# Kernel tuning notes

Hardware: AMD Instinct MI355X
Metric: run time of the kernel (lower is better)

The kernel has to match this reference:

```python
import jax, jax.numpy as jnp
import numpy as np

N_WORDS, MAX_CHARS = 32768, 16
WORD_DIM, CHAR_DIM, HIDDEN = 256, 64, 256
VOCAB = 256


def setup_inputs() -> dict:
    key = jax.random.key(0)
    ks = jax.random.split(key, 10)
    char_indices = jax.random.randint(ks[0], (N_WORDS, MAX_CHARS), 0, VOCAB)
    char_lengths = jax.random.randint(ks[1], (N_WORDS,), 1, MAX_CHARS + 1)
    word_emb = jax.random.normal(ks[2], (N_WORDS, WORD_DIM), dtype=jnp.float32)
    s = 0.05
    E_char = jax.random.normal(ks[3], (VOCAB, CHAR_DIM), dtype=jnp.float32) * s
    W_ih = jax.random.normal(ks[4], (4 * HIDDEN, CHAR_DIM), dtype=jnp.float32) * s
    W_hh = jax.random.normal(ks[5], (4 * HIDDEN, HIDDEN), dtype=jnp.float32) * s
    b_ih = jax.random.normal(ks[6], (4 * HIDDEN,), dtype=jnp.float32) * s
    b_hh = jax.random.normal(ks[7], (4 * HIDDEN,), dtype=jnp.float32) * s
    W_lin = jax.random.normal(ks[8], (WORD_DIM, WORD_DIM + HIDDEN), dtype=jnp.float32) * s
    b_lin = jax.random.normal(ks[9], (WORD_DIM,), dtype=jnp.float32) * s
    return dict(char_indices=char_indices, char_lengths=char_lengths,
                word_emb=word_emb, E_char=E_char, W_ih=W_ih, W_hh=W_hh,
                b_ih=b_ih, b_hh=b_hh, W_lin=W_lin, b_lin=b_lin)


def _lstm_last_hidden(x, lengths, W_ih, W_hh, b_ih, b_hh):
    # x: [N, T, E]; returns final hidden h at position length-1 per row.
    N, T, _ = x.shape
    H = W_hh.shape[1]
    x_proj = jnp.einsum('nte,ge->ntg', x, W_ih) + (b_ih + b_hh)  # [N, T, 4H]
    x_proj = jnp.transpose(x_proj, (1, 0, 2))                    # time-major [T, N, 4H]

    def step(carry, inp):
        h, c = carry
        xg, t = inp
        gates = xg + h @ W_hh.T
        i, f, g, o = jnp.split(gates, 4, axis=-1)
        i, f, o = jax.nn.sigmoid(i), jax.nn.sigmoid(f), jax.nn.sigmoid(o)
        g = jnp.tanh(g)
        c_new = f * c + i * g
        h_new = o * jnp.tanh(c_new)
        mask = (t < lengths)[:, None]  # freeze state past each word's length
        h = jnp.where(mask, h_new, h)
        c = jnp.where(mask, c_new, c)
        return (h, c), None

    h0 = jnp.zeros((N, H), dtype=x.dtype)
    c0 = jnp.zeros((N, H), dtype=x.dtype)
    (h, _), _ = jax.lax.scan(step, (h0, c0), (x_proj, jnp.arange(T)))
    return h


def reference(char_indices, char_lengths, word_emb, E_char, W_ih, W_hh,
              b_ih, b_hh, W_lin, b_lin):
    char_embedded = E_char[char_indices]                        # [N, T, E]
    h = _lstm_last_hidden(char_embedded, char_lengths, W_ih, W_hh, b_ih, b_hh)
    combined = jnp.concatenate([word_emb, h], axis=-1)          # [N, WORD+H]
    return jax.nn.relu(combined @ W_lin.T + b_lin)              # [N, WORD]
```

## Files before the change

### kernel.cpp

```cpp
#include <hip/hip_runtime.h>


#define NW 32768

typedef __attribute__((ext_vector_type(8))) short short8;
typedef __attribute__((ext_vector_type(4))) float f32x4;
typedef __attribute__((ext_vector_type(4))) int i32x4;
typedef __attribute__((ext_vector_type(4))) unsigned short u16x4;

#define MFMA16(a,b,c) __builtin_amdgcn_mfma_f32_16x16x32_bf16(a,b,c,0,0,0)
#define MFMAI8(a,b,c) __builtin_amdgcn_mfma_i32_16x16x32_i8(a,b,c,0,0,0)

#define O_ORDER 0
#define O_SLEN  131072
#define O_WPK   262144
#define O_USTP  524288
#define O_WLIN  528384
#define O_PX    790528
#define O_BH    1314816
#define O_BASE  1323008

__device__ inline unsigned short f2b(float f) {
  unsigned u = __builtin_bit_cast(unsigned, f);
  u = u + 0x7fffu + ((u >> 16) & 1u);
  return (unsigned short)(u >> 16);
}
__device__ inline float b2f(unsigned short u) {
  return __builtin_bit_cast(float, ((unsigned)u) << 16);
}
__device__ inline float fsigm(float x) {
  float e = __builtin_amdgcn_exp2f(-1.44269504f * x);
  return __builtin_amdgcn_rcpf(1.0f + e);
}
__device__ inline float ftanh(float x) {
  float e = __builtin_amdgcn_exp2f(2.88539008f * x);
  return 1.0f - 2.0f * __builtin_amdgcn_rcpf(e + 1.0f);
}

__global__ void k_prep0(const float* __restrict__ whh, unsigned char* __restrict__ ws) {
  int i = blockIdx.x * 256 + threadIdx.x;
  const f32x4* r4 = (const f32x4*)(whh + i * 256);
  float mx = 0.f;
  #pragma unroll 8
  for (int k4 = 0; k4 < 64; ++k4) {
    f32x4 v = r4[k4];
    mx = fmaxf(mx, fmaxf(fmaxf(fabsf(v[0]), fabsf(v[1])),
                         fmaxf(fabsf(v[2]), fabsf(v[3]))));
  }
  ((float*)(ws + O_USTP))[i] = mx / (127.f * 127.f);
}

__global__ void k_prep1(const float* __restrict__ whh, const float* __restrict__ wlin,
                        unsigned char* __restrict__ ws) {
  int i = blockIdx.x * 256 + threadIdx.x;
  if (i < 262144) {
    int j = i & 7, lane = (i >> 3) & 63, t2 = i >> 9;
    int nt = t2 & 7, u2 = t2 >> 3;
    int kb = u2 & 7, w = u2 >> 3;
    int n = (nt >> 1) * 256 + w * 32 + (nt & 1) * 16 + (lane & 15);
    int k = kb * 32 + (lane >> 4) * 8 + j;
    float v = whh[n * 256 + k];
    float ustep = ((const float*)(ws + O_USTP))[n] * 127.f;
    float qf = (ustep > 0.f) ? v / ustep : 0.f;
    int q = (int)__builtin_rintf(qf);
    q = q < -127 ? -127 : (q > 127 ? 127 : q);
    ((signed char*)(ws + O_WPK))[i] = (signed char)q;
    return;
  }
  int i2 = i - 262144;
  {
    int j = i2 & 7, lane = (i2 >> 3) & 63, t3 = i2 >> 9;
    int kf = t3 & 15, nn = t3 >> 4;
    int n = (nn >> 2) * 64 + (nn & 3) * 16 + (lane & 15);
    int k = kf * 32 + (lane >> 4) * 8 + j;
    ((unsigned short*)(ws + O_WLIN))[i2] = f2b(wlin[n * 512 + k]);
  }
}

__global__ void k_prep2(const float* __restrict__ wih, const float* __restrict__ ech,
                        const float* __restrict__ bih, const float* __restrict__ bhh,
                        unsigned char* __restrict__ ws) {
  int id = blockIdx.x * 256 + threadIdx.x;
  int c = id >> 10, n = id & 1023;
  const f32x4* w4 = (const f32x4*)(wih + n * 64);
  const f32x4* e4 = (const f32x4*)(ech + c * 64);
  float acc = bih[n] + bhh[n];
  #pragma unroll
  for (int k4 = 0; k4 < 16; ++k4) {
    f32x4 a = w4[k4], e = e4[k4];
    acc += a[0] * e[0] + a[1] * e[1] + a[2] * e[2] + a[3] * e[3];
  }
  ((unsigned short*)(ws + O_PX))[((c << 8) + (n & 255)) * 4 + (n >> 8)] = f2b(acc);
}

__global__ void k_hist(const int* __restrict__ lens, unsigned char* __restrict__ ws) {
  __shared__ int h[16];
  int t = threadIdx.x, b = blockIdx.x;
  if (t < 16) h[t] = 0;
  __syncthreads();
  int wid = b * 256 + t;
  int l = lens[wid]; l = l < 1 ? 1 : (l > 16 ? 16 : l);
  atomicAdd(&h[l - 1], 1);
  __syncthreads();
  if (t < 16) ((int*)(ws + O_BH))[b * 16 + t] = h[t];
}

__global__ void k_scan(unsigned char* __restrict__ ws) {
  __shared__ int tot[16], g[16];
  int t = threadIdx.x;
  const int* bh = (const int*)(ws + O_BH);
  int* base = (int*)(ws + O_BASE);
  if (t < 16) {
    int s = 0;
    for (int b = 0; b < 128; ++b) s += bh[b * 16 + t];
    tot[t] = s;
  }
  __syncthreads();
  if (t == 0) { int a = 0; for (int i = 0; i < 16; ++i) { g[i] = a; a += tot[i]; } }
  __syncthreads();
  if (t < 16) {
    int run = g[t];
    for (int b = 0; b < 128; ++b) { base[b * 16 + t] = run; run += bh[b * 16 + t]; }
  }
}

__global__ void k_scatter(const int* __restrict__ lens, unsigned char* __restrict__ ws) {
  __shared__ int cnt[16];
  int t = threadIdx.x, b = blockIdx.x;
  if (t < 16) cnt[t] = 0;
  __syncthreads();
  int wid = b * 256 + t;
  int l = lens[wid]; l = l < 1 ? 1 : (l > 16 ? 16 : l);
  int rank = atomicAdd(&cnt[l - 1], 1);
  int p = ((const int*)(ws + O_BASE))[b * 16 + (l - 1)] + rank;
  ((int*)(ws + O_ORDER))[p] = wid;
  ((int*)(ws + O_SLEN))[p] = l;
}

__global__ __launch_bounds__(512)
__attribute__((amdgpu_waves_per_eu(2, 2)))
void k_main(
    const int* __restrict__ cidx, const float* __restrict__ wemb,
    const float* __restrict__ blin, float* __restrict__ outp,
    const unsigned char* __restrict__ ws) {
  extern __shared__ signed char smem[];
  signed char (*WL)[8][8][64][8] = (signed char (*)[8][8][64][8])smem;
  signed char (*Xb)[8][64][8] = (signed char (*)[8][64][8])(smem + 131072);
  int (*CW)[16] = (int (*)[16])(smem + 131072 + 16384);

  const int tid = threadIdx.x, b = blockIdx.x;
  const int w = tid >> 6, lane = tid & 63;
  const int q = lane >> 4, l15 = lane & 15;

  const int* order = (const int*)(ws + O_ORDER);
  const int* slen  = (const int*)(ws + O_SLEN);
  const signed char* wpk = (const signed char*)(ws + O_WPK);
  const float* upt = (const float*)(ws + O_USTP);
  const unsigned short* wlin = (const unsigned short*)(ws + O_WLIN);
  const unsigned short* pxt = (const unsigned short*)(ws + O_PX);

  long wreg[4][8];
  #pragma unroll
  for (int kb = 0; kb < 4; ++kb)
    #pragma unroll
    for (int nt = 0; nt < 8; ++nt)
      wreg[kb][nt] = *(const long*)(wpk + (((w * 8 + kb) * 8 + nt) * 64 + lane) * 8);

  {
    long* wlds = (long*)smem;
    const long* wsrc = (const long*)wpk;
    #pragma unroll
    for (int ii = 0; ii < 32; ++ii) {
      int f = ii * 512 + tid;
      int lane_ = f & 63, r = f >> 6;
      int nt_ = r & 7, r2 = r >> 3;
      int w_ = r2 & 7, kb4 = r2 >> 3;
      wlds[f] = wsrc[((w_ * 8 + 4 + kb4) * 8 + nt_) * 64 + lane_];
    }
  }

  float uq[8];
  #pragma unroll
  for (int nt = 0; nt < 8; ++nt) {
    int n = (nt >> 1) * 256 + w * 32 + (nt & 1) * 16 + l15;
    uq[nt] = upt[n];
  }
  const int hd0 = w * 32 + l15;
  const int mh = w >> 2, nw = w & 3;
  float blv[4];
  #pragma unroll
  for (int nt = 0; nt < 4; ++nt) blv[nt] = blin[nw * 64 + nt * 16 + l15];

  for (int sl = 0; sl < 2; ++sl) {
    const int s = sl ? (511 - b) : b;
    const int base = 64 * s;
    __syncthreads();
    {
      long* p = (long*)&Xb[0][0][0][0];
      #pragma unroll
      for (int ii = 0; ii < 4; ++ii) p[tid + 512 * ii] = 0L;
    }
    if (tid < 256) {
      int m = tid >> 2, part = tid & 3;
      int wid = order[base + m];
      *(i32x4*)&CW[m][part * 4] =
          __builtin_nontemporal_load((const i32x4*)(cidx + wid * 16 + part * 4));
    }
    int tmax[4]; unsigned lenpk[4];
    #pragma unroll
    for (int mt = 0; mt < 4; ++mt) {
      int pbm = base + 16 * mt;
      tmax[mt] = slen[pbm + 15];
      unsigned l0 = (unsigned)slen[pbm + q * 4 + 0];
      unsigned l1 = (unsigned)slen[pbm + q * 4 + 1];
      unsigned l2 = (unsigned)slen[pbm + q * 4 + 2];
      unsigned l3 = (unsigned)slen[pbm + q * 4 + 3];
      lenpk[mt] = l0 | (l1 << 8) | (l2 << 16) | (l3 << 24);
    }
    const int Tm = tmax[3];
    __syncthreads();

    float creg[4][2][4];
    unsigned hreg[4][2];
    #pragma unroll
    for (int mt = 0; mt < 4; ++mt)
      #pragma unroll
      for (int hs = 0; hs < 2; ++hs) {
        hreg[mt][hs] = 0u;
        #pragma unroll
        for (int r = 0; r < 4; ++r) creg[mt][hs][r] = 0.f;
      }

    for (int t = 0; t < Tm; ++t) {
      #pragma unroll
      for (int mt = 0; mt < 4; ++mt) {
        if (mt != 3 && t >= tmax[mt]) continue;
        long Ar[8];
        #pragma unroll
        for (int kb = 0; kb < 8; ++kb)
          Ar[kb] = *(const long*)&Xb[mt][kb][lane][0];
        int cc[4];
        #pragma unroll
        for (int r = 0; r < 4; ++r) cc[r] = CW[mt * 16 + q * 4 + r][t] & 255;
        #pragma unroll
        for (int hs = 0; hs < 2; ++hs) {
          u16x4 pb[4];
          #pragma unroll
          for (int r = 0; r < 4; ++r)
            pb[r] = *(const u16x4*)&pxt[((cc[r] << 8) + hd0 + hs * 16) * 4];
          i32x4 a0 = (i32x4)0, a1 = (i32x4)0, a2 = (i32x4)0, a3 = (i32x4)0;
          #pragma unroll
          for (int kb = 0; kb < 4; ++kb) {
            a0 = MFMAI8(Ar[kb], wreg[kb][0 + hs], a0);
            a1 = MFMAI8(Ar[kb], wreg[kb][2 + hs], a1);
            a2 = MFMAI8(Ar[kb], wreg[kb][4 + hs], a2);
            a3 = MFMAI8(Ar[kb], wreg[kb][6 + hs], a3);
          }
          #pragma unroll
          for (int kb = 4; kb < 8; ++kb) {
            long b0 = *(const long*)&WL[kb - 4][w][0 + hs][lane][0];
            long b1 = *(const long*)&WL[kb - 4][w][2 + hs][lane][0];
            long b2 = *(const long*)&WL[kb - 4][w][4 + hs][lane][0];
            long b3 = *(const long*)&WL[kb - 4][w][6 + hs][lane][0];
            a0 = MFMAI8(Ar[kb], b0, a0);
            a1 = MFMAI8(Ar[kb], b1, a1);
            a2 = MFMAI8(Ar[kb], b2, a2);
            a3 = MFMAI8(Ar[kb], b3, a3);
          }
          unsigned hp = 0;
          #pragma unroll
          for (int r = 0; r < 4; ++r) {
            float gi = (float)a0[r] * uq[0 + hs] + b2f(pb[r][0]);
            float gf = (float)a1[r] * uq[2 + hs] + b2f(pb[r][1]);
            float gg = (float)a2[r] * uq[4 + hs] + b2f(pb[r][2]);
            float go = (float)a3[r] * uq[6 + hs] + b2f(pb[r][3]);
            float si = fsigm(gi), sf = fsigm(gf);
            float sg = ftanh(gg), so = fsigm(go);
            float cold = creg[mt][hs][r];
            float cn = sf * cold + si * sg;
            float hn = so * ftanh(cn);
            int lene = (int)((lenpk[mt] >> (8 * r)) & 255u);
            bool live = t < lene;
            creg[mt][hs][r] = live ? cn : cold;
            int hq = (int)__builtin_rintf(127.f * hn);
            unsigned ob = (hreg[mt][hs] >> (8 * r)) & 255u;
            unsigned nb = live ? ((unsigned)hq & 255u) : ob;
            hp |= nb << (8 * r);
          }
          hreg[mt][hs] = hp;
        }
      }
      __syncthreads();

      #pragma unroll
      for (int mt = 0; mt < 4; ++mt) {
        if (mt != 3 && t >= tmax[mt]) continue;
        #pragma unroll
        for (int hs = 0; hs < 2; ++hs) {
          int row16 = 16 * (hs * 2 + (l15 >> 3));
          #pragma unroll
          for (int r = 0; r < 4; ++r)
            Xb[mt][w][(q * 4 + r) + row16][l15 & 7] =
                (signed char)((hreg[mt][hs] >> (8 * r)) & 255u);
        }
      }
      __syncthreads();
    }

    int widA[2];
    #pragma unroll
    for (int mi = 0; mi < 2; ++mi) widA[mi] = order[base + (2 * mh + mi) * 16 + l15];
    f32x4 fac[2][4];
    #pragma unroll
    for (int mi = 0; mi < 2; ++mi)
      #pragma unroll
      for (int nt = 0; nt < 4; ++nt) fac[mi][nt] = 0.0f;

    #pragma unroll
    for (int kf = 0; kf < 16; ++kf) {
      short8 Bn[4];
      #pragma unroll
      for (int nt = 0; nt < 4; ++nt)
        Bn[nt] = ((const short8*)wlin)[((nw * 4 + nt) * 16 + kf) * 64 + lane];
      short8 Am[2];
      #pragma unroll
      for (int mi = 0; mi < 2; ++mi) {
        if (kf < 8) {
          const f32x4* pa = (const f32x4*)(wemb + widA[mi] * 256 + kf * 32 + q * 8);
          f32x4 f0 = __builtin_nontemporal_load(pa);
          f32x4 f1 = __builtin_nontemporal_load(pa + 1);
          short8 A;
          A[0] = (short)f2b(f0[0]); A[1] = (short)f2b(f0[1]);
          A[2] = (short)f2b(f0[2]); A[3] = (short)f2b(f0[3]);
          A[4] = (short)f2b(f1[0]); A[5] = (short)f2b(f1[1]);
          A[6] = (short)f2b(f1[2]); A[7] = (short)f2b(f1[3]);
          Am[mi] = A;
        } else {
          int mtv = 2 * mh + mi;
          long ch = *(const long*)&Xb[mtv][kf - 8][lane][0];
          short8 A;
          #pragma unroll
          for (int j = 0; j < 8; ++j) {
            int v = (int)(signed char)((ch >> (8 * j)) & 255);
            A[j] = (short)f2b((float)v * (1.f / 127.f));
          }
          Am[mi] = A;
        }
      }
      #pragma unroll
      for (int mi = 0; mi < 2; ++mi)
        #pragma unroll
        for (int nt = 0; nt < 4; ++nt)
          fac[mi][nt] = MFMA16(Am[mi], Bn[nt], fac[mi][nt]);
    }
    #pragma unroll
    for (int mi = 0; mi < 2; ++mi) {
      #pragma unroll
      for (int r = 0; r < 4; ++r) {
        int wid = order[base + (2 * mh + mi) * 16 + q * 4 + r];
        float* po = outp + wid * 256 + nw * 64 + l15;
        #pragma unroll
        for (int nt = 0; nt < 4; ++nt) {
          float v = fac[mi][nt][r] + blv[nt];
          __builtin_nontemporal_store(v > 0.f ? v : 0.f, po + nt * 16);
        }
      }
    }
  }
}

extern "C" void kernel_launch(void* const* d_in, const int* in_sizes, int n_in,
                              void* d_out, int out_size, void* d_ws, size_t ws_size,
                              hipStream_t stream) {
  const int*   cidx = (const int*)d_in[0];
  const int*   clen = (const int*)d_in[1];
  const float* wemb = (const float*)d_in[2];
  const float* ech  = (const float*)d_in[3];
  const float* wih  = (const float*)d_in[4];
  const float* whh  = (const float*)d_in[5];
  const float* bih  = (const float*)d_in[6];
  const float* bhh  = (const float*)d_in[7];
  const float* wlin = (const float*)d_in[8];
  const float* blin = (const float*)d_in[9];
  float* outp = (float*)d_out;
  unsigned char* ws = (unsigned char*)d_ws;

  k_prep0<<<4, 256, 0, stream>>>(whh, ws);
  k_prep1<<<1536, 256, 0, stream>>>(whh, wlin, ws);
  k_prep2<<<1024, 256, 0, stream>>>(wih, ech, bih, bhh, ws);
  k_hist<<<128, 256, 0, stream>>>(clen, ws);
  k_scan<<<1, 64, 0, stream>>>(ws);
  k_scatter<<<128, 256, 0, stream>>>(clen, ws);
  k_main<<<256, 512, 151552, stream>>>(cidx, wemb, blin, outp, ws);
}
```

Before: 399.1 us.

## Split LSTM hidden columns across 16 waves with 1024-thread blocks

Doubles the main kernel's block to 1024 threads (16 waves), with each wave handling 16 hidden units instead of 32. Per-wave recurrent weights in registers, cell state and MFMA work are halved, and the final linear layer is split so each wave handles one 16-row slice. The aim is more latency hiding in the serial recurrence. In exchange, the per-timestep barriers now synchronise more waves, and the per-step X tile is loaded from LDS by twice as many waves.

```diff
diff --git a/kernel.cpp b/kernel.cpp
--- a/kernel.cpp
+++ b/kernel.cpp
@@ -137,8 +137,7 @@
   ((int*)(ws + O_SLEN))[p] = l;
 }
 
-__global__ __launch_bounds__(512)
-__attribute__((amdgpu_waves_per_eu(2, 2)))
+__global__ __launch_bounds__(1024)
 void k_main(
     const int* __restrict__ cidx, const float* __restrict__ wemb,
     const float* __restrict__ blin, float* __restrict__ outp,
@@ -151,6 +150,7 @@
   const int tid = threadIdx.x, b = blockIdx.x;
   const int w = tid >> 6, lane = tid & 63;
   const int q = lane >> 4, l15 = lane & 15;
+  const int wo = w >> 1, wp = w & 1;
 
   const int* order = (const int*)(ws + O_ORDER);
   const int* slen  = (const int*)(ws + O_SLEN);
@@ -159,19 +159,20 @@
   const unsigned short* wlin = (const unsigned short*)(ws + O_WLIN);
   const unsigned short* pxt = (const unsigned short*)(ws + O_PX);
 
-  long wreg[4][8];
+  long wreg[4][4];
   #pragma unroll
   for (int kb = 0; kb < 4; ++kb)
     #pragma unroll
-    for (int nt = 0; nt < 8; ++nt)
-      wreg[kb][nt] = *(const long*)(wpk + (((w * 8 + kb) * 8 + nt) * 64 + lane) * 8);
+    for (int g = 0; g < 4; ++g)
+      wreg[kb][g] =
+          *(const long*)(wpk + (((wo * 8 + kb) * 8 + (2 * g + wp)) * 64 + lane) * 8);
 
   {
     long* wlds = (long*)smem;
     const long* wsrc = (const long*)wpk;
     #pragma unroll
-    for (int ii = 0; ii < 32; ++ii) {
-      int f = ii * 512 + tid;
+    for (int ii = 0; ii < 16; ++ii) {
+      int f = ii * 1024 + tid;
       int lane_ = f & 63, r = f >> 6;
       int nt_ = r & 7, r2 = r >> 3;
       int w_ = r2 & 7, kb4 = r2 >> 3;
@@ -179,17 +180,10 @@
     }
   }
 
-  float uq[8];
+  const int hd0 = w * 16 + l15;
+  float uq[4];
   #pragma unroll
-  for (int nt = 0; nt < 8; ++nt) {
-    int n = (nt >> 1) * 256 + w * 32 + (nt & 1) * 16 + l15;
-    uq[nt] = upt[n];
-  }
-  const int hd0 = w * 32 + l15;
-  const int mh = w >> 2, nw = w & 3;
-  float blv[4];
-  #pragma unroll
-  for (int nt = 0; nt < 4; ++nt) blv[nt] = blin[nw * 64 + nt * 16 + l15];
+  for (int g = 0; g < 4; ++g) uq[g] = upt[g * 256 + hd0];
 
   for (int sl = 0; sl < 2; ++sl) {
     const int s = sl ? (511 - b) : b;
@@ -197,8 +191,7 @@
     __syncthreads();
     {
       long* p = (long*)&Xb[0][0][0][0];
-      #pragma unroll
-      for (int ii = 0; ii < 4; ++ii) p[tid + 512 * ii] = 0L;
+      p[tid] = 0L; p[tid + 1024] = 0L;
     }
     if (tid < 256) {
       int m = tid >> 2, part = tid & 3;
@@ -220,150 +213,127 @@
     const int Tm = tmax[3];
     __syncthreads();
 
-    float creg[4][2][4];
-    unsigned hreg[4][2];
-    #pragma unroll
-    for (int mt = 0; mt < 4; ++mt)
-      #pragma unroll
-      for (int hs = 0; hs < 2; ++hs) {
-        hreg[mt][hs] = 0u;
-        #pragma unroll
-        for (int r = 0; r < 4; ++r) creg[mt][hs][r] = 0.f;
-      }
+    float creg[4][4];
+    unsigned hreg[4];
+    #pragma unroll
+    for (int mt = 0; mt < 4; ++mt) {
+      hreg[mt] = 0u;
+      #pragma unroll
+      for (int r = 0; r < 4; ++r) creg[mt][r] = 0.f;
+    }
 
     for (int t = 0; t < Tm; ++t) {
       #pragma unroll
       for (int mt = 0; mt < 4; ++mt) {
         if (mt != 3 && t >= tmax[mt]) continue;
-        long Ar[8];
-        #pragma unroll
-        for (int kb = 0; kb < 8; ++kb)
-          Ar[kb] = *(const long*)&Xb[mt][kb][lane][0];
         int cc[4];
         #pragma unroll
         for (int r = 0; r < 4; ++r) cc[r] = CW[mt * 16 + q * 4 + r][t] & 255;
-        #pragma unroll
-        for (int hs = 0; hs < 2; ++hs) {
-          u16x4 pb[4];
-          #pragma unroll
-          for (int r = 0; r < 4; ++r)
-            pb[r] = *(const u16x4*)&pxt[((cc[r] << 8) + hd0 + hs * 16) * 4];
-          i32x4 a0 = (i32x4)0, a1 = (i32x4)0, a2 = (i32x4)0, a3 = (i32x4)0;
-          #pragma unroll
-          for (int kb = 0; kb < 4; ++kb) {
-            a0 = MFMAI8(Ar[kb], wreg[kb][0 + hs], a0);
-            a1 = MFMAI8(Ar[kb], wreg[kb][2 + hs], a1);
-            a2 = MFMAI8(Ar[kb], wreg[kb][4 + hs], a2);
-            a3 = MFMAI8(Ar[kb], wreg[kb][6 + hs], a3);
-          }
-          #pragma unroll
-          for (int kb = 4; kb < 8; ++kb) {
-            long b0 = *(const long*)&WL[kb - 4][w][0 + hs][lane][0];
-            long b1 = *(const long*)&WL[kb - 4][w][2 + hs][lane][0];
-            long b2 = *(const long*)&WL[kb - 4][w][4 + hs][lane][0];
-            long b3 = *(const long*)&WL[kb - 4][w][6 + hs][lane][0];
-            a0 = MFMAI8(Ar[kb], b0, a0);
-            a1 = MFMAI8(Ar[kb], b1, a1);
-            a2 = MFMAI8(Ar[kb], b2, a2);
-            a3 = MFMAI8(Ar[kb], b3, a3);
-          }
-          unsigned hp = 0;
-          #pragma unroll
-          for (int r = 0; r < 4; ++r) {
-            float gi = (float)a0[r] * uq[0 + hs] + b2f(pb[r][0]);
-            float gf = (float)a1[r] * uq[2 + hs] + b2f(pb[r][1]);
-            float gg = (float)a2[r] * uq[4 + hs] + b2f(pb[r][2]);
-            float go = (float)a3[r] * uq[6 + hs] + b2f(pb[r][3]);
-            float si = fsigm(gi), sf = fsigm(gf);
-            float sg = ftanh(gg), so = fsigm(go);
-            float cold = creg[mt][hs][r];
-            float cn = sf * cold + si * sg;
-            float hn = so * ftanh(cn);
-            int lene = (int)((lenpk[mt] >> (8 * r)) & 255u);
-            bool live = t < lene;
-            creg[mt][hs][r] = live ? cn : cold;
-            int hq = (int)__builtin_rintf(127.f * hn);
-            unsigned ob = (hreg[mt][hs] >> (8 * r)) & 255u;
-            unsigned nb = live ? ((unsigned)hq & 255u) : ob;
-            hp |= nb << (8 * r);
-          }
-          hreg[mt][hs] = hp;
+        u16x4 pb[4];
+        #pragma unroll
+        for (int r = 0; r < 4; ++r)
+          pb[r] = *(const u16x4*)&pxt[((cc[r] << 8) + hd0) * 4];
+        i32x4 a0 = (i32x4)0, a1 = (i32x4)0, a2 = (i32x4)0, a3 = (i32x4)0;
+        #pragma unroll
+        for (int kb = 0; kb < 4; ++kb) {
+          long A = *(const long*)&Xb[mt][kb][lane][0];
+          a0 = MFMAI8(A, wreg[kb][0], a0);
+          a1 = MFMAI8(A, wreg[kb][1], a1);
+          a2 = MFMAI8(A, wreg[kb][2], a2);
+          a3 = MFMAI8(A, wreg[kb][3], a3);
+        }
+        #pragma unroll
+        for (int kb = 4; kb < 8; ++kb) {
+          long A = *(const long*)&Xb[mt][kb][lane][0];
+          long b0 = *(const long*)&WL[kb - 4][wo][0 + wp][lane][0];
+          long b1 = *(const long*)&WL[kb - 4][wo][2 + wp][lane][0];
+          long b2 = *(const long*)&WL[kb - 4][wo][4 + wp][lane][0];
+          long b3 = *(const long*)&WL[kb - 4][wo][6 + wp][lane][0];
+          a0 = MFMAI8(A, b0, a0);
+          a1 = MFMAI8(A, b1, a1);
+          a2 = MFMAI8(A, b2, a2);
+          a3 = MFMAI8(A, b3, a3);
+        }
+        unsigned hp = 0;
+        #pragma unroll
+        for (int r = 0; r < 4; ++r) {
+          float gi = (float)a0[r] * uq[0] + b2f(pb[r][0]);
+          float gf = (float)a1[r] * uq[1] + b2f(pb[r][1]);
+          float gg = (float)a2[r] * uq[2] + b2f(pb[r][2]);
+          float go = (float)a3[r] * uq[3] + b2f(pb[r][3]);
+          float si = fsigm(gi), sf = fsigm(gf);
+          float sg = ftanh(gg), so = fsigm(go);
+          float cold = creg[mt][r];
+          float cn = sf * cold + si * sg;
+          float hn = so * ftanh(cn);
+          int lene = (int)((lenpk[mt] >> (8 * r)) & 255u);
+          bool live = t < lene;
+          creg[mt][r] = live ? cn : cold;
+          int hq = (int)__builtin_rintf(127.f * hn);
+          unsigned ob = (hreg[mt] >> (8 * r)) & 255u;
+          unsigned nb = live ? ((unsigned)hq & 255u) : ob;
+          hp |= nb << (8 * r);
+        }
+        hreg[mt] = hp;
+      }
+      __syncthreads();
+
+      #pragma unroll
+      for (int mt = 0; mt < 4; ++mt) {
+        if (mt != 3 && t >= tmax[mt]) continue;
+        int row16 = 16 * (wp * 2 + (l15 >> 3));
+        #pragma unroll
+        for (int r = 0; r < 4; ++r)
+          Xb[mt][wo][(q * 4 + r) + row16][l15 & 7] =
+              (signed char)((hreg[mt] >> (8 * r)) & 255u);
+      }
+      __syncthreads();
+    }
+
+    const int mh2 = w >> 2, nw = w & 3;
+    float blv[4];
+    #pragma unroll
+    for (int nt = 0; nt < 4; ++nt) blv[nt] = blin[nw * 64 + nt * 16 + l15];
+    int widA = order[base + mh2 * 16 + l15];
+    f32x4 fac[4];
+    #pragma unroll
+    for (int nt = 0; nt < 4; ++nt) fac[nt] = 0.0f;
+
+    #pragma unroll
+    for (int kf = 0; kf < 16; ++kf) {
+      short8 Bn[4];
+      #pragma unroll
+      for (int nt = 0; nt < 4; ++nt)
+        Bn[nt] = ((const short8*)wlin)[((nw * 4 + nt) * 16 + kf) * 64 + lane];
+      short8 Am;
+      if (kf < 8) {
+        const f32x4* pa = (const f32x4*)(wemb + widA * 256 + kf * 32 + q * 8);
+        f32x4 f0 = __builtin_nontemporal_load(pa);
+        f32x4 f1 = __builtin_nontemporal_load(pa + 1);
+        Am[0] = (short)f2b(f0[0]); Am[1] = (short)f2b(f0[1]);
+        Am[2] = (short)f2b(f0[2]); Am[3] = (short)f2b(f0[3]);
+        Am[4] = (short)f2b(f1[0]); Am[5] = (short)f2b(f1[1]);
+        Am[6] = (short)f2b(f1[2]); Am[7] = (short)f2b(f1[3]);
+      } else {
+        long ch = *(const long*)&Xb[mh2][kf - 8][lane][0];
+        #pragma unroll
+        for (int j = 0; j < 8; ++j) {
+          int v = (int)(signed char)((ch >> (8 * j)) & 255);
+          Am[j] = (short)f2b((float)v * (1.f / 127.f));
         }
       }
-      __syncthreads();
-
-      #pragma unroll
-      for (int mt = 0; mt < 4; ++mt) {
-        if (mt != 3 && t >= tmax[mt]) continue;
-        #pragma unroll
-        for (int hs = 0; hs < 2; ++hs) {
-          int row16 = 16 * (hs * 2 + (l15 >> 3));
-          #pragma unroll
-          for (int r = 0; r < 4; ++r)
-            Xb[mt][w][(q * 4 + r) + row16][l15 & 7] =
-                (signed char)((hreg[mt][hs] >> (8 * r)) & 255u);
-        }
-      }
-      __syncthreads();
-    }
-
-    int widA[2];
-    #pragma unroll
-    for (int mi = 0; mi < 2; ++mi) widA[mi] = order[base + (2 * mh + mi) * 16 + l15];
-    f32x4 fac[2][4];
-    #pragma unroll
-    for (int mi = 0; mi < 2; ++mi)
-      #pragma unroll
-      for (int nt = 0; nt < 4; ++nt) fac[mi][nt] = 0.0f;
-
-    #pragma unroll
-    for (int kf = 0; kf < 16; ++kf) {
-      short8 Bn[4];
       #pragma unroll
       for (int nt = 0; nt < 4; ++nt)
-        Bn[nt] = ((const short8*)wlin)[((nw * 4 + nt) * 16 + kf) * 64 + lane];
-      short8 Am[2];
-      #pragma unroll
-      for (int mi = 0; mi < 2; ++mi) {
-        if (kf < 8) {
-          const f32x4* pa = (const f32x4*)(wemb + widA[mi] * 256 + kf * 32 + q * 8);
-          f32x4 f0 = __builtin_nontemporal_load(pa);
-          f32x4 f1 = __builtin_nontemporal_load(pa + 1);
-          short8 A;
-          A[0] = (short)f2b(f0[0]); A[1] = (short)f2b(f0[1]);
-          A[2] = (short)f2b(f0[2]); A[3] = (short)f2b(f0[3]);
-          A[4] = (short)f2b(f1[0]); A[5] = (short)f2b(f1[1]);
-          A[6] = (short)f2b(f1[2]); A[7] = (short)f2b(f1[3]);
-          Am[mi] = A;
-        } else {
-          int mtv = 2 * mh + mi;
-          long ch = *(const long*)&Xb[mtv][kf - 8][lane][0];
-          short8 A;
-          #pragma unroll
-          for (int j = 0; j < 8; ++j) {
-            int v = (int)(signed char)((ch >> (8 * j)) & 255);
-            A[j] = (short)f2b((float)v * (1.f / 127.f));
-          }
-          Am[mi] = A;
-        }
-      }
-      #pragma unroll
-      for (int mi = 0; mi < 2; ++mi)
-        #pragma unroll
-        for (int nt = 0; nt < 4; ++nt)
-          fac[mi][nt] = MFMA16(Am[mi], Bn[nt], fac[mi][nt]);
-    }
-    #pragma unroll
-    for (int mi = 0; mi < 2; ++mi) {
-      #pragma unroll
-      for (int r = 0; r < 4; ++r) {
-        int wid = order[base + (2 * mh + mi) * 16 + q * 4 + r];
-        float* po = outp + wid * 256 + nw * 64 + l15;
-        #pragma unroll
-        for (int nt = 0; nt < 4; ++nt) {
-          float v = fac[mi][nt][r] + blv[nt];
-          __builtin_nontemporal_store(v > 0.f ? v : 0.f, po + nt * 16);
-        }
+        fac[nt] = MFMA16(Am, Bn[nt], fac[nt]);
+    }
+    #pragma unroll
+    for (int r = 0; r < 4; ++r) {
+      int wid = order[base + mh2 * 16 + q * 4 + r];
+      float* po = outp + wid * 256 + nw * 64 + l15;
+      #pragma unroll
+      for (int nt = 0; nt < 4; ++nt) {
+        float v = fac[nt][r] + blv[nt];
+        __builtin_nontemporal_store(v > 0.f ? v : 0.f, po + nt * 16);
       }
     }
   }
@@ -391,5 +361,5 @@
   k_hist<<<128, 256, 0, stream>>>(clen, ws);
   k_scan<<<1, 64, 0, stream>>>(ws);
   k_scatter<<<128, 256, 0, stream>>>(clen, ws);
-  k_main<<<256, 512, 151552, stream>>>(cidx, wemb, blin, outp, ws);
-}
+  k_main<<<256, 1024, 151552, stream>>>(cidx, wemb, blin, outp, ws);
+}
```

Measured after the change: 475.6 us. 19.2% more time.
